# Kernel tuning notes

Measured on AMD Instinct MI355X. Metric: run time of the kernel, lower is better.

The kernel has to match this reference:

```python
import jax, jax.numpy as jnp
import numpy as np

HEADS = 8   # from init_kwargs
K_SIZE = 64

def setup_inputs() -> dict:
    key = jax.random.key(0)
    k1, k2, k3, k4 = jax.random.split(key, 4)
    B, C, D = 4, 2048, 1024
    return {
        "x": jax.random.normal(k1, (B, C, D), dtype=jnp.float32),
        "Mq": jax.random.normal(k2, (D, HEADS * K_SIZE), dtype=jnp.float32) * 0.02,
        "Mk": jax.random.normal(k3, (D, HEADS * K_SIZE), dtype=jnp.float32) * 0.02,
        "Mv": jax.random.normal(k4, (D, 1024), dtype=jnp.float32) * 0.02,
    }

def reference(x, Mq, Mk, Mv):
    B, C, _ = x.shape
    H, K = HEADS, K_SIZE
    V = Mv.shape[1] // H  # v_size = output_size // heads = 128
    # Faithful to torch: (x @ M).view(B, H, C, -1) is a raw row-major reshape
    # of the [B, C, H*K] projection, which mixes token and head axes exactly
    # as the original module does.
    q = (x @ Mq).reshape(B, H, C, K)
    k = (x @ Mk).reshape(B, H, C, K)
    v = (x @ Mv).reshape(B, H, C, V)
    # scores: [B*H, C, C]; scale by sqrt(k_size); softmax over dim=1 (the
    # first C axis), matching the original's unusual softmax dim.
    scores = jnp.einsum('bhqk,bhck->bhqc', q, k).reshape(B * H, C, C)
    att = jax.nn.softmax(scores / jnp.sqrt(jnp.float32(K)), axis=1)
    # att_weights.view(B, C, heads, -1): raw reshape from [B*H, C, C]
    att4 = att.reshape(B, C, H, C)
    # intended semantics of `att4 @ v`: per-head attn-weighted sum of values
    out = jnp.einsum('bqhc,bhcd->bqhd', att4, v)  # [B, C, H, V]
    return out.reshape(B, C, H * V)
```

## Files before the change

### kernel.cpp

```cpp
#include <hip/hip_runtime.h>
#include <stdint.h>
#include <stddef.h>


typedef short     bf8v  __attribute__((ext_vector_type(8)));
typedef float     f4v   __attribute__((ext_vector_type(4)));
typedef unsigned short u16x4 __attribute__((ext_vector_type(4)));
typedef unsigned short u16x8 __attribute__((ext_vector_type(8)));

__device__ __forceinline__ unsigned short f2bf(float f) {
    union { float f; uint32_t u; } v; v.f = f;
    return (unsigned short)((v.u + 0x7fffu + ((v.u >> 16) & 1u)) >> 16);
}

#define MFMA32(A, B, C) __builtin_amdgcn_mfma_f32_16x16x32_bf16((A), (B), (C), 0, 0, 0)
#define ASYNC16(g, l) __builtin_amdgcn_global_load_lds(                        \
    (const __attribute__((address_space(1))) unsigned int*)(g),                \
    (__attribute__((address_space(3))) unsigned int*)(l), 16, 0, 0)

__global__ __launch_bounds__(256) void k_cvt(const float* __restrict__ in,
                                             unsigned short* __restrict__ out, int n4) {
    int i = blockIdx.x * 256 + threadIdx.x;
    if (i >= n4) return;
    f4v v = *(const f4v*)(in + (size_t)i * 4);
    u16x4 o;
    o[0] = f2bf(v[0]); o[1] = f2bf(v[1]); o[2] = f2bf(v[2]); o[3] = f2bf(v[3]);
    *(u16x4*)(out + (size_t)i * 4) = o;
}

__global__ __launch_bounds__(256) void k_cvtT3(const float* __restrict__ Mq,
                                               const float* __restrict__ Mk,
                                               const float* __restrict__ Mv,
                                               unsigned short* __restrict__ wqt,
                                               unsigned short* __restrict__ wkt,
                                               unsigned short* __restrict__ wvt) {
    __shared__ unsigned short t[64][68];
    const int tid = threadIdx.x;
    const int tr = tid >> 4, tc4 = (tid & 15) * 4;
    const float* in; unsigned short* outT; int Ncols, cb;
    if (blockIdx.z == 0) {
        if (blockIdx.x < 8) { in = Mq; outT = wqt; Ncols = 512; cb = blockIdx.x * 64; }
        else                { in = Mk; outT = wkt; Ncols = 512; cb = (blockIdx.x - 8) * 64; }
    } else                  { in = Mv; outT = wvt; Ncols = 1024; cb = blockIdx.x * 64; }
    const int rb = blockIdx.y * 64;
#pragma unroll
    for (int p = 0; p < 4; ++p) {
        int r = tr + p * 16;
        f4v v = *(const f4v*)(in + (size_t)(rb + r) * Ncols + cb + tc4);
        t[r][tc4 + 0] = f2bf(v[0]); t[r][tc4 + 1] = f2bf(v[1]);
        t[r][tc4 + 2] = f2bf(v[2]); t[r][tc4 + 3] = f2bf(v[3]);
    }
    __syncthreads();
#pragma unroll
    for (int p = 0; p < 4; ++p) {
        int r = tr + p * 16;
        u16x4 o;
        o[0] = t[tc4 + 0][r]; o[1] = t[tc4 + 1][r];
        o[2] = t[tc4 + 2][r]; o[3] = t[tc4 + 3][r];
        *(u16x4*)(outT + (size_t)(cb + r) * 1024 + rb + tc4) = o;
    }
}

__global__ __launch_bounds__(256) void k_T(const unsigned short* __restrict__ in,
                                           unsigned short* __restrict__ out) {
    __shared__ unsigned short t[64][68];
    const int tid = threadIdx.x;
    const int tr = tid >> 4, tc4 = (tid & 15) * 4;
    const int rb = blockIdx.y * 64, cb = blockIdx.x * 64;
    const unsigned short* ib = in  + (size_t)blockIdx.z * 262144;
    unsigned short*       ob = out + (size_t)blockIdx.z * 262144;
#pragma unroll
    for (int p = 0; p < 4; ++p) {
        int r = tr + p * 16;
        u16x4 v = *(const u16x4*)(ib + (size_t)(rb + r) * 128 + cb + tc4);
        t[r][tc4 + 0] = v[0]; t[r][tc4 + 1] = v[1];
        t[r][tc4 + 2] = v[2]; t[r][tc4 + 3] = v[3];
    }
    __syncthreads();
#pragma unroll
    for (int p = 0; p < 4; ++p) {
        int r = tr + p * 16;
        u16x4 o;
        o[0] = t[tc4 + 0][r]; o[1] = t[tc4 + 1][r];
        o[2] = t[tc4 + 2][r]; o[3] = t[tc4 + 3][r];
        *(u16x4*)(ob + (size_t)(cb + r) * 2048 + rb + tc4) = o;
    }
}

__global__ __launch_bounds__(256, 2) void k_gemm(const unsigned short* __restrict__ X,
                                                 const unsigned short* __restrict__ Wt,
                                                 unsigned short* __restrict__ pq,
                                                 unsigned short* __restrict__ pk,
                                                 unsigned short* __restrict__ pv) {
    __shared__ __align__(16) unsigned short xs[2][8192];
    __shared__ __align__(16) unsigned short ws2[2][8192];
    const int tid = threadIdx.x;
    const int lane = tid & 63, w = tid >> 6;
    const int lc = lane & 15, quad = lane >> 4;
    const int rowb = blockIdx.x * 128, cb = blockIdx.y;

    unsigned short* outp; int N, colb; float scale;
    if (cb < 4)      { outp = pq; N = 512;  colb = cb * 128;       scale = 0.125f; }
    else if (cb < 8) { outp = pk; N = 512;  colb = (cb - 4) * 128; scale = 1.0f; }
    else             { outp = pv; N = 1024; colb = (cb - 8) * 128; scale = 1.0f; }

    const int lr   = lane >> 3;
    const int swz  = ((lane & 7) ^ lr) * 8;

    f4v acc[2][8];
#pragma unroll
    for (int mt = 0; mt < 2; ++mt)
#pragma unroll
        for (int nt = 0; nt < 8; ++nt) acc[mt][nt] = f4v{0.f, 0.f, 0.f, 0.f};

#pragma unroll
    for (int j = 0; j < 4; ++j) {
        int row = (w * 4 + j) * 8 + lr;
        ASYNC16(X  + (size_t)(rowb + row) * 1024 + swz,            &xs[0][(w * 4 + j) * 512]);
        ASYNC16(Wt + (size_t)(cb * 128 + row) * 1024 + swz,        &ws2[0][(w * 4 + j) * 512]);
    }
    __syncthreads();

    for (int k = 0; k < 16; ++k) {
        const int buf = k & 1;
        if (k < 15) {
            const int k0n = (k + 1) * 64;
#pragma unroll
            for (int j = 0; j < 4; ++j) {
                int row = (w * 4 + j) * 8 + lr;
                ASYNC16(X  + (size_t)(rowb + row) * 1024 + k0n + swz,     &xs[buf ^ 1][(w * 4 + j) * 512]);
                ASYNC16(Wt + (size_t)(cb * 128 + row) * 1024 + k0n + swz, &ws2[buf ^ 1][(w * 4 + j) * 512]);
            }
        }
#pragma unroll
        for (int ks = 0; ks < 2; ++ks) {
            bf8v bx[8];
#pragma unroll
            for (int nt = 0; nt < 8; ++nt) {
                int row = nt * 16 + lc;
                int c8  = (ks * 4 + quad) ^ (lc & 7);
                bx[nt] = *(const bf8v*)(&xs[buf][row * 64 + c8 * 8]);
            }
#pragma unroll
            for (int mt = 0; mt < 2; ++mt) {
                int row = w * 32 + mt * 16 + lc;
                int c8  = (ks * 4 + quad) ^ (lc & 7);
                bf8v a = *(const bf8v*)(&ws2[buf][row * 64 + c8 * 8]);
#pragma unroll
                for (int nt = 0; nt < 8; ++nt) acc[mt][nt] = MFMA32(a, bx[nt], acc[mt][nt]);
            }
        }
        __syncthreads();
    }
#pragma unroll
    for (int mt = 0; mt < 2; ++mt)
#pragma unroll
        for (int nt = 0; nt < 8; ++nt) {
            int crow = rowb + nt * 16 + lc;
            int ccol = colb + w * 32 + mt * 16 + quad * 4;
            u16x4 o;
            o[0] = f2bf(acc[mt][nt][0] * scale); o[1] = f2bf(acc[mt][nt][1] * scale);
            o[2] = f2bf(acc[mt][nt][2] * scale); o[3] = f2bf(acc[mt][nt][3] * scale);
            *(u16x4*)(outp + (size_t)crow * N + ccol) = o;
        }
}

__global__ __launch_bounds__(256, 2) void k_pass1(const unsigned short* __restrict__ Pq,
                                                  const unsigned short* __restrict__ Pk,
                                                  float* __restrict__ rdenl) {
    __shared__ __align__(16) unsigned short kls[8192];
    __shared__ __align__(16) unsigned short qls[2][8192];
    __shared__ float dsum[4][128];
    const int tid = threadIdx.x;
    const int lane = tid & 63, w = tid >> 6;
    const int lc = lane & 15, quad = lane >> 4;
    const int c2b = blockIdx.x * 128;
    const int bg  = blockIdx.y;
    const unsigned short* qbase = Pq + (size_t)bg * 131072;
    const unsigned short* kbase = Pk + (size_t)bg * 131072 + (size_t)c2b * 64;

    const int lr  = lane >> 3;
    const int swz = ((lane & 7) ^ lr) * 8;

#pragma unroll
    for (int j = 0; j < 4; ++j) {
        int row = (w * 4 + j) * 8 + lr;
        ASYNC16(kbase + (size_t)row * 64 + swz, &kls[(w * 4 + j) * 512]);
        ASYNC16(qbase + (size_t)row * 64 + swz, &qls[0][(w * 4 + j) * 512]);
    }
    __syncthreads();

    float csum[8];
#pragma unroll
    for (int nt = 0; nt < 8; ++nt) csum[nt] = 0.f;

    for (int it = 0; it < 16; ++it) {
        const int buf = it & 1;
        if (it < 15) {
            const unsigned short* qn = qbase + (size_t)(it + 1) * 8192;
#pragma unroll
            for (int j = 0; j < 4; ++j) {
                int row = (w * 4 + j) * 8 + lr;
                ASYNC16(qn + (size_t)row * 64 + swz, &qls[buf ^ 1][(w * 4 + j) * 512]);
            }
        }

        f4v sc[2][8];
#pragma unroll
        for (int mt = 0; mt < 2; ++mt)
#pragma unroll
            for (int nt = 0; nt < 8; ++nt) sc[mt][nt] = f4v{0.f, 0.f, 0.f, 0.f};
#pragma unroll
        for (int ks = 0; ks < 2; ++ks) {
            bf8v bk[8];
#pragma unroll
            for (int nt = 0; nt < 8; ++nt) {
                int row = nt * 16 + lc;
                int c8  = (ks * 4 + quad) ^ (lc & 7);
                bk[nt] = *(const bf8v*)(&kls[row * 64 + c8 * 8]);
            }
#pragma unroll
            for (int mt = 0; mt < 2; ++mt) {
                int row = w * 32 + mt * 16 + lc;
                int c8  = (ks * 4 + quad) ^ (lc & 7);
                bf8v a = *(const bf8v*)(&qls[buf][row * 64 + c8 * 8]);
#pragma unroll
                for (int nt = 0; nt < 8; ++nt) sc[mt][nt] = MFMA32(a, bk[nt], sc[mt][nt]);
            }
        }
#pragma unroll
        for (int mt = 0; mt < 2; ++mt)
#pragma unroll
            for (int nt = 0; nt < 8; ++nt)
#pragma unroll
                for (int r = 0; r < 4; ++r)
                    csum[nt] += __expf(sc[mt][nt][r]);
        __syncthreads();
    }

#pragma unroll
    for (int nt = 0; nt < 8; ++nt) {
        float v = csum[nt];
        v += __shfl_xor(v, 16, 64);
        v += __shfl_xor(v, 32, 64);
        if (quad == 0) dsum[w][nt * 16 + lc] = v;
    }
    __syncthreads();
    if (tid < 128) {
        float tot = dsum[0][tid] + dsum[1][tid] + dsum[2][tid] + dsum[3][tid];
        rdenl[(size_t)bg * 2048 + c2b + tid] = -__logf(tot);
    }
}

__global__ __launch_bounds__(256, 2) void k_pass2(const unsigned short* __restrict__ Pq,
                                                  const unsigned short* __restrict__ Pk,
                                                  const unsigned short* __restrict__ Vt,
                                                  const float* __restrict__ rdenl,
                                                  float* __restrict__ out) {
    __shared__ __align__(16) unsigned short qs[128][72];
    __shared__ __align__(16) unsigned short kss[2][64][72];
    __shared__ __align__(16) unsigned short vs[2][128][72];
    const int tid = threadIdx.x;
    const int lane = tid & 63, w = tid >> 6;
    const int lc = lane & 15, quad = lane >> 4;
    const int jt = blockIdx.x, h = blockIdx.y, bg = blockIdx.z;
    const int b = bg >> 3, g = bg & 7;

    const unsigned short* qbase = Pq + (size_t)bg * 131072;
    const unsigned short* kbase = Pk + (size_t)bg * 131072;
    const unsigned short* vbase = Vt + (size_t)(b * 8 + h) * 262144;
    const float* rdl = rdenl + (size_t)bg * 2048;

#pragma unroll
    for (int p = 0; p < 4; ++p) {
        int v = tid + p * 256;
        int i = v >> 3, s = (v & 7) * 8;
        *(u16x8*)(&qs[i][s]) =
            *(const u16x8*)(qbase + (size_t)((jt * 128 + i) * 8 + h) * 64 + s);
    }
#pragma unroll
    for (int p = 0; p < 2; ++p) {
        int v = tid + p * 256;
        int c8 = ((v & 7) + (v >> 6)) & 7;
        *(u16x8*)(&kss[0][v >> 3][c8 * 8]) = *(const u16x8*)(kbase + (size_t)v * 8);
    }
#pragma unroll
    for (int p = 0; p < 4; ++p) {
        int v = tid + p * 256;
        int d = v >> 3, s = (v & 7) * 8;
        *(u16x8*)(&vs[0][d][s]) = *(const u16x8*)(vbase + (size_t)d * 2048 + s);
    }
    __syncthreads();

    bf8v bq[2][2];
#pragma unroll
    for (int nt = 0; nt < 2; ++nt)
#pragma unroll
        for (int ks = 0; ks < 2; ++ks)
            bq[nt][ks] = *(const bf8v*)(&qs[w * 32 + nt * 16 + lc][ks * 32 + quad * 8]);

    f4v acc[8][2];
#pragma unroll
    for (int dt = 0; dt < 8; ++dt)
#pragma unroll
        for (int nt = 0; nt < 2; ++nt) acc[dt][nt] = f4v{0.f, 0.f, 0.f, 0.f};

    for (int cc = 0; cc < 32; ++cc) {
        const int buf = cc & 1;
        u16x8 kreg[2], vreg[4];
        if (cc < 31) {
            const int c2n = (cc + 1) * 64;
#pragma unroll
            for (int p = 0; p < 2; ++p) {
                int v = tid + p * 256;
                kreg[p] = *(const u16x8*)(kbase + (size_t)c2n * 64 + (size_t)v * 8);
            }
#pragma unroll
            for (int p = 0; p < 4; ++p) {
                int v = tid + p * 256;
                vreg[p] = *(const u16x8*)(vbase + (size_t)(v >> 3) * 2048 + c2n + (v & 7) * 8);
            }
        }

        f4v sc[4][2];
#pragma unroll
        for (int mt = 0; mt < 4; ++mt)
#pragma unroll
            for (int nt = 0; nt < 2; ++nt) sc[mt][nt] = f4v{0.f, 0.f, 0.f, 0.f};
#pragma unroll
        for (int ks = 0; ks < 2; ++ks) {
            bf8v a[4];
#pragma unroll
            for (int mt = 0; mt < 4; ++mt) {
                int rlog = ((mt >> 1) << 5) + ((lc >> 2) << 3) + ((mt & 1) << 2) + (lc & 3);
                int c8   = ((ks << 2) + quad + ((mt >> 1) << 2) + (lc >> 2)) & 7;
                a[mt] = *(const bf8v*)(&kss[buf][rlog][c8 * 8]);
            }
#pragma unroll
            for (int mt = 0; mt < 4; ++mt)
#pragma unroll
                for (int nt = 0; nt < 2; ++nt)
                    sc[mt][nt] = MFMA32(a[mt], bq[nt][ks], sc[mt][nt]);
        }

        bf8v pb[2][2];
#pragma unroll
        for (int mt = 0; mt < 4; ++mt) {
            f4v lrd = *(const f4v*)(rdl + cc * 64 + ((mt >> 1) << 5) + (quad << 3) + ((mt & 1) << 2));
#pragma unroll
            for (int nt = 0; nt < 2; ++nt)
#pragma unroll
                for (int i = 0; i < 4; ++i)
                    pb[mt >> 1][nt][(mt & 1) * 4 + i] =
                        (short)f2bf(__expf(sc[mt][nt][i] + lrd[i]));
        }

#pragma unroll
        for (int kc = 0; kc < 2; ++kc)
#pragma unroll
            for (int dt = 0; dt < 8; ++dt) {
                bf8v a = *(const bf8v*)(&vs[buf][dt * 16 + lc][kc * 32 + quad * 8]);
#pragma unroll
                for (int nt = 0; nt < 2; ++nt)
                    acc[dt][nt] = MFMA32(a, pb[kc][nt], acc[dt][nt]);
            }

        if (cc < 31) {
            const int nbuf = buf ^ 1;
#pragma unroll
            for (int p = 0; p < 2; ++p) {
                int v = tid + p * 256;
                int c8 = ((v & 7) + (v >> 6)) & 7;
                *(u16x8*)(&kss[nbuf][v >> 3][c8 * 8]) = kreg[p];
            }
#pragma unroll
            for (int p = 0; p < 4; ++p) {
                int v = tid + p * 256;
                *(u16x8*)(&vs[nbuf][v >> 3][(v & 7) * 8]) = vreg[p];
            }
        }
        __syncthreads();
    }

    float* ob = out + (size_t)(b * 2048 + g * 256 + jt * 128) * 1024 + h * 128;
#pragma unroll
    for (int dt = 0; dt < 8; ++dt)
#pragma unroll
        for (int nt = 0; nt < 2; ++nt) {
            int r = w * 32 + nt * 16 + lc;
            int d = dt * 16 + quad * 4;
            *(f4v*)(ob + (size_t)r * 1024 + d) = acc[dt][nt];
        }
}

extern "C" void kernel_launch(void* const* d_in, const int* in_sizes, int n_in,
                              void* d_out, int out_size, void* d_ws, size_t ws_size,
                              hipStream_t stream) {
    const float* x  = (const float*)d_in[0];
    const float* Mq = (const float*)d_in[1];
    const float* Mk = (const float*)d_in[2];
    const float* Mv = (const float*)d_in[3];
    float* out = (float*)d_out;

    char* base = (char*)d_ws;
    unsigned short* xb  = (unsigned short*)base;  base += 16777216;
    unsigned short* wqt = (unsigned short*)base;  base += 1048576;
    unsigned short* wkt = (unsigned short*)base;  base += 1048576;
    unsigned short* wvt = (unsigned short*)base;  base += 2097152;
    unsigned short* pq  = (unsigned short*)base;  base += 8388608;
    unsigned short* pk  = (unsigned short*)base;  base += 8388608;
    unsigned short* pv  = (unsigned short*)base;  base += 16777216;
    unsigned short* vt  = (unsigned short*)base;  base += 16777216;
    float* rdenl = (float*)base;                  base += 262144;

    k_cvt<<<8192, 256, 0, stream>>>(x, xb, 2097152);
    k_cvtT3<<<dim3(16, 16, 2), 256, 0, stream>>>(Mq, Mk, Mv, wqt, wkt, wvt);
    k_gemm<<<dim3(64, 16), 256, 0, stream>>>(xb, wqt , pq, pk, pv);
    k_T<<<dim3(2, 32, 32), 256, 0, stream>>>(pv, vt);
    k_pass1<<<dim3(16, 32), 256, 0, stream>>>(pq, pk, rdenl);
    k_pass2<<<dim3(2, 8, 32), 256, 0, stream>>>(pq, pk, vt, rdenl, out);
}
```

Baseline: 230.4 us.

## Use async global-to-LDS loads in pass2 and packed bf16 conversion

The pass2 kernel's K/V tiles are now streamed straight into LDS with global_load_lds instead of being loaded into registers and stored to shared memory. The tiles use unpadded, XOR/rotation-swizzled layouts, and Q fragments are read directly from global memory instead of through a shared staging buffer. Float-to-bf16 conversion is changed everywhere to a two-value packed round-half-up via byte permute, replacing per-element round-to-nearest-even. This aims to cut register pressure, VALU work and LDS staging, but it slightly changes rounding and relies on the new swizzle math being correct.

```diff
diff --git a/kernel.cpp b/kernel.cpp
--- a/kernel.cpp
+++ b/kernel.cpp
@@ -7,10 +7,11 @@
 typedef float     f4v   __attribute__((ext_vector_type(4)));
 typedef unsigned short u16x4 __attribute__((ext_vector_type(4)));
 typedef unsigned short u16x8 __attribute__((ext_vector_type(8)));
-
-__device__ __forceinline__ unsigned short f2bf(float f) {
-    union { float f; uint32_t u; } v; v.f = f;
-    return (unsigned short)((v.u + 0x7fffu + ((v.u >> 16) & 1u)) >> 16);
+typedef unsigned int   u32x4 __attribute__((ext_vector_type(4)));
+
+__device__ __forceinline__ unsigned int pk2(float a, float b) {
+    union { float f; uint32_t u; } x, y; x.f = a; y.f = b;
+    return __builtin_amdgcn_perm(y.u + 0x8000u, x.u + 0x8000u, 0x07060302u);
 }
 
 #define MFMA32(A, B, C) __builtin_amdgcn_mfma_f32_16x16x32_bf16((A), (B), (C), 0, 0, 0)
@@ -23,9 +24,8 @@
     int i = blockIdx.x * 256 + threadIdx.x;
     if (i >= n4) return;
     f4v v = *(const f4v*)(in + (size_t)i * 4);
-    u16x4 o;
-    o[0] = f2bf(v[0]); o[1] = f2bf(v[1]); o[2] = f2bf(v[2]); o[3] = f2bf(v[3]);
-    *(u16x4*)(out + (size_t)i * 4) = o;
+    uint2 o; o.x = pk2(v[0], v[1]); o.y = pk2(v[2], v[3]);
+    *(uint2*)(out + (size_t)i * 4) = o;
 }
 
 __global__ __launch_bounds__(256) void k_cvtT3(const float* __restrict__ Mq,
@@ -47,8 +47,8 @@
     for (int p = 0; p < 4; ++p) {
         int r = tr + p * 16;
         f4v v = *(const f4v*)(in + (size_t)(rb + r) * Ncols + cb + tc4);
-        t[r][tc4 + 0] = f2bf(v[0]); t[r][tc4 + 1] = f2bf(v[1]);
-        t[r][tc4 + 2] = f2bf(v[2]); t[r][tc4 + 3] = f2bf(v[3]);
+        *(unsigned int*)&t[r][tc4]     = pk2(v[0], v[1]);
+        *(unsigned int*)&t[r][tc4 + 2] = pk2(v[2], v[3]);
     }
     __syncthreads();
 #pragma unroll
@@ -92,8 +92,7 @@
                                                  unsigned short* __restrict__ pq,
                                                  unsigned short* __restrict__ pk,
                                                  unsigned short* __restrict__ pv) {
-    __shared__ __align__(16) unsigned short xs[2][8192];
-    __shared__ __align__(16) unsigned short ws2[2][8192];
+    __shared__ __align__(16) unsigned short smem[32768];
     const int tid = threadIdx.x;
     const int lane = tid & 63, w = tid >> 6;
     const int lc = lane & 15, quad = lane >> 4;
@@ -116,20 +115,22 @@
 #pragma unroll
     for (int j = 0; j < 4; ++j) {
         int row = (w * 4 + j) * 8 + lr;
-        ASYNC16(X  + (size_t)(rowb + row) * 1024 + swz,            &xs[0][(w * 4 + j) * 512]);
-        ASYNC16(Wt + (size_t)(cb * 128 + row) * 1024 + swz,        &ws2[0][(w * 4 + j) * 512]);
+        ASYNC16(X  + (size_t)(rowb + row) * 1024 + swz,     &smem[(w * 4 + j) * 512]);
+        ASYNC16(Wt + (size_t)(cb * 128 + row) * 1024 + swz, &smem[16384 + (w * 4 + j) * 512]);
     }
     __syncthreads();
 
     for (int k = 0; k < 16; ++k) {
         const int buf = k & 1;
+        const int xoff = buf * 8192, woff = 16384 + buf * 8192;
         if (k < 15) {
             const int k0n = (k + 1) * 64;
+            const int nx = (buf ^ 1) * 8192, nw = 16384 + (buf ^ 1) * 8192;
 #pragma unroll
             for (int j = 0; j < 4; ++j) {
                 int row = (w * 4 + j) * 8 + lr;
-                ASYNC16(X  + (size_t)(rowb + row) * 1024 + k0n + swz,     &xs[buf ^ 1][(w * 4 + j) * 512]);
-                ASYNC16(Wt + (size_t)(cb * 128 + row) * 1024 + k0n + swz, &ws2[buf ^ 1][(w * 4 + j) * 512]);
+                ASYNC16(X  + (size_t)(rowb + row) * 1024 + k0n + swz,     &smem[nx + (w * 4 + j) * 512]);
+                ASYNC16(Wt + (size_t)(cb * 128 + row) * 1024 + k0n + swz, &smem[nw + (w * 4 + j) * 512]);
             }
         }
 #pragma unroll
@@ -139,13 +140,13 @@
             for (int nt = 0; nt < 8; ++nt) {
                 int row = nt * 16 + lc;
                 int c8  = (ks * 4 + quad) ^ (lc & 7);
-                bx[nt] = *(const bf8v*)(&xs[buf][row * 64 + c8 * 8]);
+                bx[nt] = *(const bf8v*)(&smem[xoff + row * 64 + c8 * 8]);
             }
 #pragma unroll
             for (int mt = 0; mt < 2; ++mt) {
                 int row = w * 32 + mt * 16 + lc;
                 int c8  = (ks * 4 + quad) ^ (lc & 7);
-                bf8v a = *(const bf8v*)(&ws2[buf][row * 64 + c8 * 8]);
+                bf8v a = *(const bf8v*)(&smem[woff + row * 64 + c8 * 8]);
 #pragma unroll
                 for (int nt = 0; nt < 8; ++nt) acc[mt][nt] = MFMA32(a, bx[nt], acc[mt][nt]);
             }
@@ -158,10 +159,10 @@
         for (int nt = 0; nt < 8; ++nt) {
             int crow = rowb + nt * 16 + lc;
             int ccol = colb + w * 32 + mt * 16 + quad * 4;
-            u16x4 o;
-            o[0] = f2bf(acc[mt][nt][0] * scale); o[1] = f2bf(acc[mt][nt][1] * scale);
-            o[2] = f2bf(acc[mt][nt][2] * scale); o[3] = f2bf(acc[mt][nt][3] * scale);
-            *(u16x4*)(outp + (size_t)crow * N + ccol) = o;
+            uint2 o;
+            o.x = pk2(acc[mt][nt][0] * scale, acc[mt][nt][1] * scale);
+            o.y = pk2(acc[mt][nt][2] * scale, acc[mt][nt][3] * scale);
+            *(uint2*)(outp + (size_t)crow * N + ccol) = o;
         }
 }
 
@@ -257,9 +258,8 @@
                                                   const unsigned short* __restrict__ Vt,
                                                   const float* __restrict__ rdenl,
                                                   float* __restrict__ out) {
-    __shared__ __align__(16) unsigned short qs[128][72];
-    __shared__ __align__(16) unsigned short kss[2][64][72];
-    __shared__ __align__(16) unsigned short vs[2][128][72];
+    __shared__ __align__(16) unsigned short kss[2][4096];
+    __shared__ __align__(16) unsigned short vs[2][8192];
     const int tid = threadIdx.x;
     const int lane = tid & 63, w = tid >> 6;
     const int lc = lane & 15, quad = lane >> 4;
@@ -271,33 +271,30 @@
     const unsigned short* vbase = Vt + (size_t)(b * 8 + h) * 262144;
     const float* rdl = rdenl + (size_t)bg * 2048;
 
-#pragma unroll
-    for (int p = 0; p < 4; ++p) {
-        int v = tid + p * 256;
-        int i = v >> 3, s = (v & 7) * 8;
-        *(u16x8*)(&qs[i][s]) =
-            *(const u16x8*)(qbase + (size_t)((jt * 128 + i) * 8 + h) * 64 + s);
-    }
-#pragma unroll
-    for (int p = 0; p < 2; ++p) {
-        int v = tid + p * 256;
-        int c8 = ((v & 7) + (v >> 6)) & 7;
-        *(u16x8*)(&kss[0][v >> 3][c8 * 8]) = *(const u16x8*)(kbase + (size_t)v * 8);
-    }
-#pragma unroll
-    for (int p = 0; p < 4; ++p) {
-        int v = tid + p * 256;
-        int d = v >> 3, s = (v & 7) * 8;
-        *(u16x8*)(&vs[0][d][s]) = *(const u16x8*)(vbase + (size_t)d * 2048 + s);
-    }
-    __syncthreads();
-
     bf8v bq[2][2];
 #pragma unroll
     for (int nt = 0; nt < 2; ++nt)
 #pragma unroll
         for (int ks = 0; ks < 2; ++ks)
-            bq[nt][ks] = *(const bf8v*)(&qs[w * 32 + nt * 16 + lc][ks * 32 + quad * 8]);
+            bq[nt][ks] = *(const bf8v*)(qbase +
+                (size_t)((jt * 128 + w * 32 + nt * 16 + lc) * 8 + h) * 64 + ks * 32 + quad * 8);
+
+    const int l3 = lane >> 3, l7 = lane & 7;
+#pragma unroll
+    for (int j = 0; j < 2; ++j) {
+        int seg = w * 2 + j;
+        int r   = seg * 8 + l3;
+        int c   = (l7 - seg - 2 * (l3 & 3)) & 7;
+        ASYNC16(kbase + (size_t)r * 64 + c * 8, &kss[0][seg * 512]);
+    }
+#pragma unroll
+    for (int j = 0; j < 4; ++j) {
+        int seg = w * 4 + j;
+        int d   = seg * 8 + l3;
+        int c   = (l7 - l3) & 7;
+        ASYNC16(vbase + (size_t)d * 2048 + c * 8, &vs[0][seg * 512]);
+    }
+    __syncthreads();
 
     f4v acc[8][2];
 #pragma unroll
@@ -307,18 +304,21 @@
 
     for (int cc = 0; cc < 32; ++cc) {
         const int buf = cc & 1;
-        u16x8 kreg[2], vreg[4];
         if (cc < 31) {
             const int c2n = (cc + 1) * 64;
 #pragma unroll
-            for (int p = 0; p < 2; ++p) {
-                int v = tid + p * 256;
-                kreg[p] = *(const u16x8*)(kbase + (size_t)c2n * 64 + (size_t)v * 8);
-            }
-#pragma unroll
-            for (int p = 0; p < 4; ++p) {
-                int v = tid + p * 256;
-                vreg[p] = *(const u16x8*)(vbase + (size_t)(v >> 3) * 2048 + c2n + (v & 7) * 8);
+            for (int j = 0; j < 2; ++j) {
+                int seg = w * 2 + j;
+                int r   = seg * 8 + l3;
+                int c   = (l7 - seg - 2 * (l3 & 3)) & 7;
+                ASYNC16(kbase + (size_t)(c2n + r) * 64 + c * 8, &kss[buf ^ 1][seg * 512]);
+            }
+#pragma unroll
+            for (int j = 0; j < 4; ++j) {
+                int seg = w * 4 + j;
+                int d   = seg * 8 + l3;
+                int c   = (l7 - l3) & 7;
+                ASYNC16(vbase + (size_t)d * 2048 + c2n + c * 8, &vs[buf ^ 1][seg * 512]);
             }
         }
 
@@ -333,8 +333,8 @@
 #pragma unroll
             for (int mt = 0; mt < 4; ++mt) {
                 int rlog = ((mt >> 1) << 5) + ((lc >> 2) << 3) + ((mt & 1) << 2) + (lc & 3);
-                int c8   = ((ks << 2) + quad + ((mt >> 1) << 2) + (lc >> 2)) & 7;
-                a[mt] = *(const bf8v*)(&kss[buf][rlog][c8 * 8]);
+                int slot = (ks * 4 + quad + ((mt >> 1) << 2) + (lc >> 2) + 2 * (lc & 3)) & 7;
+                a[mt] = *(const bf8v*)(&kss[buf][rlog * 64 + slot * 8]);
             }
 #pragma unroll
             for (int mt = 0; mt < 4; ++mt)
@@ -343,42 +343,32 @@
                     sc[mt][nt] = MFMA32(a[mt], bq[nt][ks], sc[mt][nt]);
         }
 
-        bf8v pb[2][2];
+        u32x4 pb[2][2];
 #pragma unroll
         for (int mt = 0; mt < 4; ++mt) {
             f4v lrd = *(const f4v*)(rdl + cc * 64 + ((mt >> 1) << 5) + (quad << 3) + ((mt & 1) << 2));
 #pragma unroll
-            for (int nt = 0; nt < 2; ++nt)
-#pragma unroll
-                for (int i = 0; i < 4; ++i)
-                    pb[mt >> 1][nt][(mt & 1) * 4 + i] =
-                        (short)f2bf(__expf(sc[mt][nt][i] + lrd[i]));
+            for (int nt = 0; nt < 2; ++nt) {
+                float e0 = __expf(sc[mt][nt][0] + lrd[0]);
+                float e1 = __expf(sc[mt][nt][1] + lrd[1]);
+                float e2 = __expf(sc[mt][nt][2] + lrd[2]);
+                float e3 = __expf(sc[mt][nt][3] + lrd[3]);
+                pb[mt >> 1][nt][(mt & 1) * 2 + 0] = pk2(e0, e1);
+                pb[mt >> 1][nt][(mt & 1) * 2 + 1] = pk2(e2, e3);
+            }
         }
 
 #pragma unroll
         for (int kc = 0; kc < 2; ++kc)
 #pragma unroll
             for (int dt = 0; dt < 8; ++dt) {
-                bf8v a = *(const bf8v*)(&vs[buf][dt * 16 + lc][kc * 32 + quad * 8]);
+                int dd = dt * 16 + lc;
+                int slot = (kc * 4 + quad + (lc & 7)) & 7;
+                bf8v a = *(const bf8v*)(&vs[buf][dd * 64 + slot * 8]);
 #pragma unroll
                 for (int nt = 0; nt < 2; ++nt)
-                    acc[dt][nt] = MFMA32(a, pb[kc][nt], acc[dt][nt]);
-            }
-
-        if (cc < 31) {
-            const int nbuf = buf ^ 1;
-#pragma unroll
-            for (int p = 0; p < 2; ++p) {
-                int v = tid + p * 256;
-                int c8 = ((v & 7) + (v >> 6)) & 7;
-                *(u16x8*)(&kss[nbuf][v >> 3][c8 * 8]) = kreg[p];
-            }
-#pragma unroll
-            for (int p = 0; p < 4; ++p) {
-                int v = tid + p * 256;
-                *(u16x8*)(&vs[nbuf][v >> 3][(v & 7) * 8]) = vreg[p];
-            }
-        }
+                    acc[dt][nt] = MFMA32(a, *(const bf8v*)&pb[kc][nt], acc[dt][nt]);
+            }
         __syncthreads();
     }
 
```

Result: slower. 247.9 us (+7.6%).
